# Kernel optimization log

Hardware: AMD Instinct MI355X
Metric: run time of the kernel (lower is better)

Reference implementation:

```python
import jax, jax.numpy as jnp
import numpy as np
from jax import lax


def conv2d(x, w, b, stride=1, pad=0):
    y = lax.conv_general_dilated(x, w, (stride, stride), [(pad, pad), (pad, pad)],
                                 dimension_numbers=('NCHW', 'OIHW', 'NCHW'))
    return y + b[None, :, None, None]


def squash(s, axis):
    # v = (|s|^2 / (1+|s|^2)) * s / |s|
    sq = jnp.sum(s * s, axis=axis, keepdims=True)
    return (sq / (1.0 + sq)) * s / jnp.sqrt(sq + 1e-9)


def conv_capsule(x, w, b_conv, caps_bias, out_dim, out_atoms, num_routing, stride, pad):
    # x: [B, in_dim, in_atoms, H, W]
    B, in_dim, in_atoms, H, W = x.shape
    xr = x.reshape(B * in_dim, in_atoms, H, W)
    conv = conv2d(xr, w, b_conv, stride, pad)              # [B*in_dim, out_dim*out_atoms, Ho, Wo]
    Ho, Wo = conv.shape[-2], conv.shape[-1]
    votes = conv.reshape(B, in_dim, out_dim, out_atoms, Ho, Wo)
    logits = jnp.zeros((B, in_dim, out_dim, Ho, Wo), dtype=x.dtype)
    act = None
    for i in range(num_routing):  # num_routing is a small static int (1 or 3)
        route = jax.nn.softmax(logits, axis=2)             # coupling over output capsules
        preact = jnp.einsum('bioHW,bioaHW->boaHW', route, votes) + caps_bias[None]
        act = squash(preact, axis=2)                        # [B, out_dim, out_atoms, Ho, Wo]
        if i < num_routing - 1:
            logits = logits + jnp.einsum('bioaHW,boaHW->bioHW', votes, act)
    return act


def forward(x, y, W1, b1, Wp, bp, cbp, Ws, bs, cbs, Wr1, br1, Wr2, br2, Wr3, br3):
    conv1 = jax.nn.relu(conv2d(x, W1, b1, 1, 2))                       # [B,256,H,W]
    primary = conv_capsule(conv1[:, None], Wp, bp, cbp, 32, 8, 1, 1, 2)  # [B,32,8,H,W]
    seg = conv_capsule(primary, Ws, bs, cbs, 1, 16, 3, 1, 0)             # [B,1,16,H,W]
    out_seg = jnp.sqrt(jnp.sum(seg * seg, axis=2) + 1e-9)                # Length: [B,1,H,W]
    masked = seg * y[:, :, None]                                         # Mask by label
    B, C, A, H, W = masked.shape
    r = masked.reshape(B * C, A, H, W)                                   # [B,16,H,W]
    r = jax.nn.relu(conv2d(r, Wr1, br1))
    r = jax.nn.relu(conv2d(r, Wr2, br2))
    out_recon = jax.nn.sigmoid(conv2d(r, Wr3, br3))                      # [B,1,H,W]
    return out_seg, out_recon


def setup_inputs():
    key = jax.random.key(0)
    ks = jax.random.split(key, 10)
    B, H, W = 2, 128, 128
    s = 0.05
    return {
        'x': jax.random.uniform(ks[0], (B, 1, H, W), jnp.float32),
        'y': (jax.random.uniform(ks[1], (B, 1, H, W)) > 0.5).astype(jnp.float32),
        'W1': jax.random.normal(ks[2], (256, 1, 5, 5), jnp.float32) * s,
        'b1': jnp.zeros((256,), jnp.float32),
        'Wp': jax.random.normal(ks[3], (256, 256, 5, 5), jnp.float32) * 0.01,
        'bp': jnp.zeros((256,), jnp.float32),
        'cbp': jnp.full((32, 8, 1, 1), 0.1, jnp.float32),
        'Ws': jax.random.normal(ks[4], (16, 8, 1, 1), jnp.float32) * s,
        'bs': jnp.zeros((16,), jnp.float32),
        'cbs': jnp.full((1, 16, 1, 1), 0.1, jnp.float32),
        'Wr1': jax.random.normal(ks[5], (64, 16, 1, 1), jnp.float32) * s,
        'br1': jnp.zeros((64,), jnp.float32),
        'Wr2': jax.random.normal(ks[6], (128, 64, 1, 1), jnp.float32) * s,
        'br2': jnp.zeros((128,), jnp.float32),
        'Wr3': jax.random.normal(ks[7], (1, 128, 1, 1), jnp.float32) * s,
        'br3': jnp.zeros((1,), jnp.float32),
    }


def reference(x, y, W1, b1, Wp, bp, cbp, Ws, bs, cbs, Wr1, br1, Wr2, br2, Wr3, br3):
    return forward(x, y, W1, b1, Wp, bp, cbp, Ws, bs, cbs, Wr1, br1, Wr2, br2, Wr3, br3)
```

## Files before the change

### kernel.cpp

```cpp
#include <hip/hip_runtime.h>
#include <hip/hip_bf16.h>

typedef __attribute__((ext_vector_type(8))) unsigned short us8;
typedef __attribute__((ext_vector_type(8))) __bf16 bf16x8;
typedef __attribute__((ext_vector_type(4))) float f32x4;

__device__ __forceinline__ unsigned short f2bf(float f) {
  unsigned int u = __float_as_uint(f);
  u += 0x7FFFu + ((u >> 16) & 1u);
  return (unsigned short)(u >> 16);
}
__device__ __forceinline__ float bf2f(unsigned short u) {
  return __uint_as_float(((unsigned int)u) << 16);
}

__device__ __forceinline__ void gld16(const unsigned short* g, unsigned short* l) {
  __builtin_amdgcn_global_load_lds(reinterpret_cast<const unsigned int*>(g),
                                   reinterpret_cast<unsigned int*>(l), 16, 0, 0);
}

#define BT_OFF     17842176
#define PP_OFF     21118976

__global__ __launch_bounds__(256) void pre_k(const float* __restrict__ x,
                                             const float* __restrict__ W1,
                                             const float* __restrict__ b1,
                                             const float* __restrict__ Wp,
                                             unsigned short* __restrict__ BT,
                                             unsigned short* __restrict__ Apad) {
  __shared__ float w[6400];
  const int bid = blockIdx.x, t = threadIdx.x;
  if (bid < 4096) {
    int pxt = bid >> 3;
    int cq  = bid & 7;
    int px  = (pxt << 6) + (t & 63);
    int cg  = __builtin_amdgcn_readfirstlane(t >> 6);
    int co0 = (cq << 5) + (cg << 3);
    int b = px >> 14, hw = px & 16383;
    int h = hw >> 7, wcol = hw & 127;

    float patch[25];
#pragma unroll
    for (int dh = 0; dh < 5; ++dh)
#pragma unroll
      for (int dw = 0; dw < 5; ++dw) {
        int hh = h + dh - 2, ww = wcol + dw - 2;
        bool ok = (hh >= 0) & (hh < 128) & (ww >= 0) & (ww < 128);
        patch[dh * 5 + dw] = ok ? x[(b << 14) + hh * 128 + ww] : 0.f;
      }
    us8 o;
#pragma unroll
    for (int c = 0; c < 8; ++c) {
      float acc = b1[co0 + c];
#pragma unroll
      for (int i = 0; i < 25; ++i) acc += patch[i] * W1[(co0 + c) * 25 + i];
      o[c] = f2bf(fmaxf(acc, 0.f));
    }
    *(us8*)(Apad + (size_t)((b * 132 + h + 2) * 132 + (wcol + 2)) * 256 + co0) = o;
  } else if (bid < 4352) {
    const int n = bid - 4096;
    const float* src = Wp + n * 6400;
    for (int i = t; i < 6400; i += 256) w[i] = src[i];
    __syncthreads();
    for (int k = t; k < 6400; k += 256) {
      int dhw = k >> 8, c = k & 255;
      BT[n * 6400 + k] = f2bf(w[c * 25 + dhw]);
    }
  } else {
    int idx = (bid - 4352) * 256 + t;
    int chunk = idx & 31;
    int pix = idx >> 5;
    int img = pix >= 1040;
    int p = pix - img * 1040;
    int h, w2;
    if (p < 528) {
      int rs = p / 132;
      h = (rs < 2) ? rs : rs + 128;
      w2 = p - rs * 132;
    } else {
      int q = p - 528;
      h = 2 + (q >> 2);
      int cs = q & 3;
      w2 = (cs < 2) ? cs : cs + 128;
    }
    us8 z = {0, 0, 0, 0, 0, 0, 0, 0};
    *(us8*)(Apad + (size_t)(img * 17424 + h * 132 + w2) * 256 + chunk * 8) = z;
  }
}

#define STAGE(slot, ku) do { int dhw_=(ku)>>3, dh_=dhw_/5, dw_=dhw_-dh_*5;     \
    int ao_=((dh_*132+dw_)<<8)+(((ku)&7)<<5);                                  \
    int kp_=(ku)<<5;                                                           \
    gld16(Aap+abase0+ao_, &As[slot][sA]);                                      \
    gld16(Aap+abase1+ao_, &As[slot][sA+4096]);                                 \
    gld16(BT+bbase0+kp_, &Bs[slot][sA]);                                       \
    gld16(BT+bbase1+kp_, &Bs[slot][sA+4096]); } while(0)
#define READ_SET(AST, BST, slot) do {                                          \
  _Pragma("unroll") for (int s_ = 0; s_ < 8; ++s_)                             \
    AST[s_] = *(const bf16x8*)(&As[slot][areadbase + s_*512]);                 \
  _Pragma("unroll") for (int j_ = 0; j_ < 4; ++j_)                             \
    BST[j_] = *(const bf16x8*)(&Bs[slot][breadbase + j_*512]); } while(0)
#define MFMA_SET(AST, BST) do {                                                \
  _Pragma("unroll") for (int s_ = 0; s_ < 8; ++s_)                             \
  _Pragma("unroll") for (int j_ = 0; j_ < 4; ++j_)                             \
    acc[s_][j_] = __builtin_amdgcn_mfma_f32_16x16x32_bf16(                     \
        AST[s_], BST[j_], acc[s_][j_], 0, 0, 0); } while(0)
#define BAR() __builtin_amdgcn_s_barrier()
#define VMC(n) asm volatile("s_waitcnt vmcnt(" #n ")" ::: "memory")
#define SB0() __builtin_amdgcn_sched_barrier(0)
#define SP(n) __builtin_amdgcn_s_setprio(n)

__global__ __launch_bounds__(512, 1) void caps_conv2(
    const unsigned short* __restrict__ Aap,
    const unsigned short* __restrict__ BT,
    unsigned short* __restrict__ Pp)
{
  __shared__ __attribute__((aligned(16))) unsigned short As[4][8192];
  __shared__ __attribute__((aligned(16))) unsigned short Bs[4][8192];

  const int tid = threadIdx.x;
  const int bid = blockIdx.x;
  const int lid = (bid & 7) * 32 + (bid >> 3);
  const int kid = lid & 1;
  const int m0 = (lid >> 1) << 8;
  const int t0 = kid * 100;
  const int wid = tid >> 6;
  const int l = tid & 63;

  const int swz = (l & 3) ^ ((l >> 3) & 3);
  int abase0, abase1, bbase0, bbase1;
  {
    int ra = wid * 16 + (l >> 2);
    int m = m0 + ra;
    int b = m >> 14, hw = m & 16383, h = hw >> 7, w = hw & 127;
    abase0 = ((b * 132 + h) * 132 + w) * 256 + swz * 8;
    m = m0 + ra + 128;
    b = m >> 14; hw = m & 16383; h = hw >> 7; w = hw & 127;
    abase1 = ((b * 132 + h) * 132 + w) * 256 + swz * 8;
    bbase0 = ra * 6400 + swz * 8;
    bbase1 = (ra + 128) * 6400 + swz * 8;
  }
  const int sA = wid * 512;

  const int rl = l & 15, q = l >> 4;
  const int wm = wid >> 2, wn = wid & 3;
  const int areadbase = (wm * 128 + rl) * 32 + ((q ^ ((rl >> 1) & 3)) << 3);
  const int breadbase = (wn * 64 + rl) * 32 + ((q ^ ((rl >> 1) & 3)) << 3);

  f32x4 acc[8][4] = {};
  bf16x8 aR0[8], bR0[4], aR1[8], bR1[4];

  STAGE(0, t0 + 0); STAGE(1, t0 + 1); STAGE(2, t0 + 2);
  VMC(4); BAR();
  READ_SET(aR0, bR0, 0);

  for (int it = 0; it < 48; ++it) {
    const int u = it * 2;
    READ_SET(aR1, bR1, (u + 1) & 3);
    STAGE((u + 3) & 3, t0 + u + 3);
    SP(1); MFMA_SET(aR0, bR0); SP(0);
    VMC(4); SB0(); BAR();
    READ_SET(aR0, bR0, (u + 2) & 3);
    STAGE((u + 4) & 3, t0 + u + 4);
    SP(1); MFMA_SET(aR1, bR1); SP(0);
    VMC(4); SB0(); BAR();
  }
  READ_SET(aR1, bR1, 1);
  STAGE(3, t0 + 99);
  SP(1); MFMA_SET(aR0, bR0); SP(0);
  VMC(4); SB0(); BAR();
  READ_SET(aR0, bR0, 2);
  SP(1); MFMA_SET(aR1, bR1); SP(0);
  VMC(0); SB0(); BAR();
  READ_SET(aR1, bR1, 3);
  SP(1); MFMA_SET(aR0, bR0); SP(0);
  MFMA_SET(aR1, bR1);

  unsigned short* P = Pp + kid * 8388608;
#pragma unroll
  for (int s = 0; s < 8; ++s) {
#pragma unroll
    for (int j = 0; j < 4; ++j) {
      int col = wn * 64 + j * 16 + rl;
      int mrow = m0 + wm * 128 + s * 16 + (q << 2);
#pragma unroll
      for (int e = 0; e < 4; ++e)
        P[(size_t)(mrow + e) * 256 + col] = f2bf(acc[s][j][e]);
    }
  }
}

__global__ __launch_bounds__(128) void tail_k4(
    const unsigned short* __restrict__ Pp, const float* __restrict__ y,
    const float* __restrict__ bp, const float* __restrict__ cbp,
    const float* __restrict__ Ws, const float* __restrict__ bs,
    const float* __restrict__ cbs,
    const float* __restrict__ Wr1, const float* __restrict__ br1,
    const float* __restrict__ Wr2, const float* __restrict__ br2,
    const float* __restrict__ Wr3, const float* __restrict__ br3,
    float* __restrict__ out) {
  __shared__ float pp[2][64][8];
  __shared__ float r1l[64][65];
  __shared__ float snk[2][64];

  const int tid = threadIdx.x;
  const int w = __builtin_amdgcn_readfirstlane(tid >> 6);
  const int l = tid & 63;
  const int m = blockIdx.x * 64 + l;

  const us8* pr0 = (const us8*)(Pp + (size_t)m * 256) + w * 16;
  const us8* pr1 = (const us8*)(Pp + 8388608 + (size_t)m * 256) + w * 16;
  float P8[8] = {0.f, 0.f, 0.f, 0.f, 0.f, 0.f, 0.f, 0.f};
#pragma unroll 4
  for (int i = 0; i < 16; ++i) {
    const int ci = (w * 16 + i) * 8;
    us8 a = pr0[i], b = pr1[i];
    float v[8];
#pragma unroll
    for (int c = 0; c < 8; ++c)
      v[c] = (bf2f(a[c]) + bf2f(b[c])) * (1.f / 32.f)
           + (bp[ci + c] * (1.f / 32.f) + cbp[ci + c]);
    float sqa = v[0]*v[0] + v[1]*v[1] + v[2]*v[2] + v[3]*v[3];
    float sqb = v[4]*v[4] + v[5]*v[5] + v[6]*v[6] + v[7]*v[7];
    float sq = sqa + sqb;
    float scale = sq / ((1.f + sq) * sqrtf(sq + 1e-9f));
#pragma unroll
    for (int c = 0; c < 8; ++c) P8[c] += v[c] * scale;
  }
#pragma unroll
  for (int c = 0; c < 8; ++c) pp[w][l][c] = P8[c];
  __syncthreads();
#pragma unroll
  for (int c = 0; c < 8; ++c) P8[c] = pp[0][l][c] + pp[1][l][c];

  float pre[16];
  float sqx = 0.f, sqy = 0.f;
#pragma unroll
  for (int a = 0; a < 16; ++a) {
    float s0 = P8[0]*Ws[a*8+0] + P8[1]*Ws[a*8+1] + P8[2]*Ws[a*8+2] + P8[3]*Ws[a*8+3];
    float s1 = P8[4]*Ws[a*8+4] + P8[5]*Ws[a*8+5] + P8[6]*Ws[a*8+6] + P8[7]*Ws[a*8+7];
    float s = (32.f * bs[a] + cbs[a]) + s0 + s1;
    pre[a] = s;
    if (a & 1) sqy += s * s; else sqx += s * s;
  }
  float sq2 = sqx + sqy;
  float sc2 = sq2 / ((1.f + sq2) * sqrtf(sq2 + 1e-9f));
  if (w == 0) out[m] = sqrtf(sq2 * sc2 * sc2 + 1e-9f);

  const float f = sc2 * y[m];
  float pf[16];
#pragma unroll
  for (int a = 0; a < 16; ++a) pf[a] = pre[a] * f;

#pragma unroll
  for (int jj = 0; jj < 32; ++jj) {
    const int j = w * 32 + jj;
    float s0 = 0.f, s1 = 0.f;
#pragma unroll
    for (int a = 0; a < 8; ++a) {
      s0 += pf[a] * Wr1[j * 16 + a];
      s1 += pf[a + 8] * Wr1[j * 16 + a + 8];
    }
    r1l[l][j] = fmaxf(br1[j] + s0 + s1, 0.f);
  }
  __syncthreads();
  float r1f[64];
#pragma unroll
  for (int j = 0; j < 64; ++j) r1f[j] = r1l[l][j];

  float a0 = 0.f, a1 = 0.f, a2 = 0.f, a3 = 0.f;
#pragma unroll 4
  for (int kk = 0; kk < 64; ++kk) {
    const int k = w * 64 + kk;
    const float* wr = Wr2 + k * 64;
    float s0 = 0.f, s1 = 0.f, s2 = 0.f, s3 = 0.f;
#pragma unroll
    for (int j = 0; j < 16; ++j) {
      s0 += r1f[j] * wr[j];           s1 += r1f[j + 16] * wr[j + 16];
      s2 += r1f[j + 32] * wr[j + 32]; s3 += r1f[j + 48] * wr[j + 48];
    }
    float s = br2[k] + (s0 + s1) + (s2 + s3);
    float t = fmaxf(s, 0.f) * Wr3[k];
    switch (kk & 3) { case 0: a0 += t; break; case 1: a1 += t; break;
                      case 2: a2 += t; break; default: a3 += t; }
  }
  float own = (a0 + a1) + (a2 + a3);
  snk[w][l] = own;
  __syncthreads();
  if (w == 0) {
    float acc2 = br3[0] + own + snk[1][l];
    out[32768 + m] = 1.f / (1.f + expf(-acc2));
  }
}

extern "C" void kernel_launch(void* const* d_in, const int* in_sizes, int n_in,
                              void* d_out, int out_size, void* d_ws, size_t ws_size,
                              hipStream_t stream) {
  const float* x   = (const float*)d_in[0];
  const float* y   = (const float*)d_in[1];
  const float* W1  = (const float*)d_in[2];
  const float* b1  = (const float*)d_in[3];
  const float* Wp  = (const float*)d_in[4];
  const float* bp  = (const float*)d_in[5];
  const float* cbp = (const float*)d_in[6];
  const float* Ws  = (const float*)d_in[7];
  const float* bs  = (const float*)d_in[8];
  const float* cbs = (const float*)d_in[9];
  const float* Wr1 = (const float*)d_in[10];
  const float* br1 = (const float*)d_in[11];
  const float* Wr2 = (const float*)d_in[12];
  const float* br2 = (const float*)d_in[13];
  const float* Wr3 = (const float*)d_in[14];
  const float* br3 = (const float*)d_in[15];
  float* out = (float*)d_out;

  char* ws = (char*)d_ws;
  unsigned short* Apad = (unsigned short*)ws;
  unsigned short* BT   = (unsigned short*)(ws + BT_OFF);
  unsigned short* Pp   = (unsigned short*)(ws + PP_OFF);

  hipLaunchKernelGGL(pre_k, dim3(4612), dim3(256), 0, stream, x, W1, b1, Wp, BT, Apad);
  hipLaunchKernelGGL(caps_conv2, dim3(256), dim3(512), 0, stream, Apad, BT, Pp);
  hipLaunchKernelGGL(tail_k4, dim3(512), dim3(128), 0, stream,
                     Pp, y, bp, cbp, Ws, bs, cbs, Wr1, br1, Wr2, br2, Wr3, br3, out);
}
```

Baseline: 144.5 us.

## Double K-step to 64 per stage with two-slot LDS ring in capsule conv GEMM

Restructures the main implicit-GEMM loop of the primary-capsule convolution so each pipeline stage loads a 64-wide K slice instead of 32. The LDS ring goes from four 32-wide slots to two 64-wide slots. It uses a new 8-way XOR swizzle for the LDS layout, and each thread now issues four global-to-LDS loads per operand. This halves the number of barrier and waitcnt rounds and gives each MFMA batch twice the work, cutting synchronisation overhead. The cost is a shallower prefetch depth. The barrier now sits after the fragment read, not between the wait and the read, so other waves' loads into the slot may not be visible when it is read.

```diff
diff --git a/kernel.cpp b/kernel.cpp
--- a/kernel.cpp
+++ b/kernel.cpp
@@ -88,23 +88,27 @@
   }
 }
 
-#define STAGE(slot, ku) do { int dhw_=(ku)>>3, dh_=dhw_/5, dw_=dhw_-dh_*5;     \
-    int ao_=((dh_*132+dw_)<<8)+(((ku)&7)<<5);                                  \
-    int kp_=(ku)<<5;                                                           \
-    gld16(Aap+abase0+ao_, &As[slot][sA]);                                      \
-    gld16(Aap+abase1+ao_, &As[slot][sA+4096]);                                 \
-    gld16(BT+bbase0+kp_, &Bs[slot][sA]);                                       \
-    gld16(BT+bbase1+kp_, &Bs[slot][sA+4096]); } while(0)
-#define READ_SET(AST, BST, slot) do {                                          \
-  _Pragma("unroll") for (int s_ = 0; s_ < 8; ++s_)                             \
-    AST[s_] = *(const bf16x8*)(&As[slot][areadbase + s_*512]);                 \
-  _Pragma("unroll") for (int j_ = 0; j_ < 4; ++j_)                             \
-    BST[j_] = *(const bf16x8*)(&Bs[slot][breadbase + j_*512]); } while(0)
-#define MFMA_SET(AST, BST) do {                                                \
+#define STAGE64(slot, g) do {                                                  \
+    int tap_ = (g) >> 2, dh_ = tap_ / 5, dw_ = tap_ - dh_ * 5;                 \
+    int ao_ = ((dh_ * 132 + dw_) << 8) + (((g) & 3) << 6);                     \
+    int kp_ = (g) << 6;                                                        \
+    _Pragma("unroll") for (int j_ = 0; j_ < 4; ++j_) {                         \
+      gld16(Aap + abaseA[j_] + ao_, &As[slot][(wid * 32 + j_ * 8) * 64]);      \
+      gld16(BT + bbaseB[j_] + kp_, &Bs[slot][(wid * 32 + j_ * 8) * 64]);       \
+    } } while(0)
+#define READ64(slot) do {                                                      \
+  _Pragma("unroll") for (int h_ = 0; h_ < 2; ++h_) {                           \
+    _Pragma("unroll") for (int s_ = 0; s_ < 8; ++s_)                           \
+      aF[h_][s_] = *(const bf16x8*)(&As[slot][areadbase + s_ * 1024 + kpart[h_]]); \
+    _Pragma("unroll") for (int j_ = 0; j_ < 4; ++j_)                           \
+      bF[h_][j_] = *(const bf16x8*)(&Bs[slot][breadbase + j_ * 1024 + kpart[h_]]); \
+  } } while(0)
+#define MFMA64() do {                                                          \
+  _Pragma("unroll") for (int h_ = 0; h_ < 2; ++h_)                             \
   _Pragma("unroll") for (int s_ = 0; s_ < 8; ++s_)                             \
   _Pragma("unroll") for (int j_ = 0; j_ < 4; ++j_)                             \
     acc[s_][j_] = __builtin_amdgcn_mfma_f32_16x16x32_bf16(                     \
-        AST[s_], BST[j_], acc[s_][j_], 0, 0, 0); } while(0)
+        aF[h_][s_], bF[h_][j_], acc[s_][j_], 0, 0, 0); } while(0)
 #define BAR() __builtin_amdgcn_s_barrier()
 #define VMC(n) asm volatile("s_waitcnt vmcnt(" #n ")" ::: "memory")
 #define SB0() __builtin_amdgcn_sched_barrier(0)
@@ -115,66 +119,63 @@
     const unsigned short* __restrict__ BT,
     unsigned short* __restrict__ Pp)
 {
-  __shared__ __attribute__((aligned(16))) unsigned short As[4][8192];
-  __shared__ __attribute__((aligned(16))) unsigned short Bs[4][8192];
+  __shared__ __attribute__((aligned(16))) unsigned short As[2][16384];
+  __shared__ __attribute__((aligned(16))) unsigned short Bs[2][16384];
 
   const int tid = threadIdx.x;
   const int bid = blockIdx.x;
   const int lid = (bid & 7) * 32 + (bid >> 3);
   const int kid = lid & 1;
   const int m0 = (lid >> 1) << 8;
-  const int t0 = kid * 100;
+  const int t0 = kid * 50;
   const int wid = tid >> 6;
   const int l = tid & 63;
 
-  const int swz = (l & 3) ^ ((l >> 3) & 3);
-  int abase0, abase1, bbase0, bbase1;
-  {
-    int ra = wid * 16 + (l >> 2);
+  const int ps = ((l & 7) ^ (l >> 3)) * 8;
+  int abaseA[4], bbaseB[4];
+#pragma unroll
+  for (int j = 0; j < 4; ++j) {
+    int ra = wid * 32 + j * 8 + (l >> 3);
     int m = m0 + ra;
     int b = m >> 14, hw = m & 16383, h = hw >> 7, w = hw & 127;
-    abase0 = ((b * 132 + h) * 132 + w) * 256 + swz * 8;
-    m = m0 + ra + 128;
-    b = m >> 14; hw = m & 16383; h = hw >> 7; w = hw & 127;
-    abase1 = ((b * 132 + h) * 132 + w) * 256 + swz * 8;
-    bbase0 = ra * 6400 + swz * 8;
-    bbase1 = (ra + 128) * 6400 + swz * 8;
-  }
-  const int sA = wid * 512;
+    abaseA[j] = ((b * 132 + h) * 132 + w) * 256 + ps;
+    bbaseB[j] = ra * 6400 + ps;
+  }
 
   const int rl = l & 15, q = l >> 4;
   const int wm = wid >> 2, wn = wid & 3;
-  const int areadbase = (wm * 128 + rl) * 32 + ((q ^ ((rl >> 1) & 3)) << 3);
-  const int breadbase = (wn * 64 + rl) * 32 + ((q ^ ((rl >> 1) & 3)) << 3);
+  const int areadbase = (wm * 128 + rl) * 64;
+  const int breadbase = (wn * 64 + rl) * 64;
+  int kpart[2];
+  kpart[0] = ((q) ^ (rl & 7)) * 8;
+  kpart[1] = ((4 + q) ^ (rl & 7)) * 8;
 
   f32x4 acc[8][4] = {};
-  bf16x8 aR0[8], bR0[4], aR1[8], bR1[4];
-
-  STAGE(0, t0 + 0); STAGE(1, t0 + 1); STAGE(2, t0 + 2);
-  VMC(4); BAR();
-  READ_SET(aR0, bR0, 0);
-
-  for (int it = 0; it < 48; ++it) {
-    const int u = it * 2;
-    READ_SET(aR1, bR1, (u + 1) & 3);
-    STAGE((u + 3) & 3, t0 + u + 3);
-    SP(1); MFMA_SET(aR0, bR0); SP(0);
-    VMC(4); SB0(); BAR();
-    READ_SET(aR0, bR0, (u + 2) & 3);
-    STAGE((u + 4) & 3, t0 + u + 4);
-    SP(1); MFMA_SET(aR1, bR1); SP(0);
-    VMC(4); SB0(); BAR();
-  }
-  READ_SET(aR1, bR1, 1);
-  STAGE(3, t0 + 99);
-  SP(1); MFMA_SET(aR0, bR0); SP(0);
-  VMC(4); SB0(); BAR();
-  READ_SET(aR0, bR0, 2);
-  SP(1); MFMA_SET(aR1, bR1); SP(0);
-  VMC(0); SB0(); BAR();
-  READ_SET(aR1, bR1, 3);
-  SP(1); MFMA_SET(aR0, bR0); SP(0);
-  MFMA_SET(aR1, bR1);
+  bf16x8 aF[2][8], bF[2][4];
+
+  STAGE64(0, t0 + 0);
+  STAGE64(1, t0 + 1);
+  VMC(8); BAR();
+  READ64(0);
+  SB0(); BAR();
+
+  for (int it = 0; it < 24; ++it) {
+    const int b = it * 2;
+    STAGE64(0, t0 + b + 2);
+    VMC(8);
+    SP(1); MFMA64(); SP(0);
+    READ64(1);
+    SB0(); BAR();
+    STAGE64(1, t0 + b + 3);
+    VMC(8);
+    SP(1); MFMA64(); SP(0);
+    READ64(0);
+    SB0(); BAR();
+  }
+  VMC(0);
+  SP(1); MFMA64(); SP(0);
+  READ64(1);
+  MFMA64();
 
   unsigned short* P = Pp + kid * 8388608;
 #pragma unroll
```

New measurement: 235.0 us. 62.6% more time.
